# Kernel tuning notes

Measured on AMD Instinct MI355X. Metric: run time of the kernel, lower is better.

Reference implementation:

```python
import jax, jax.numpy as jnp
import numpy as np

M, IN, H, OUT, B = 64, 64, 256, 1, 4096


def setup_inputs() -> dict:
    key = jax.random.key(0)
    ks = jax.random.split(key, 7)
    s1 = 1.0 / np.sqrt(IN)
    s2 = 1.0 / np.sqrt(H)
    return {
        "xs": jax.random.normal(ks[0], (M, B, IN), dtype=jnp.float32),
        "W1": jax.random.uniform(ks[1], (M, IN, H), minval=-s1, maxval=s1, dtype=jnp.float32),
        "b1": jax.random.uniform(ks[2], (M, H), minval=-s1, maxval=s1, dtype=jnp.float32),
        "W2": jax.random.uniform(ks[3], (M, H, H), minval=-s2, maxval=s2, dtype=jnp.float32),
        "b2": jax.random.uniform(ks[4], (M, H), minval=-s2, maxval=s2, dtype=jnp.float32),
        "W3": jax.random.uniform(ks[5], (M, H, OUT), minval=-s2, maxval=s2, dtype=jnp.float32),
        "b3": jax.random.uniform(ks[6], (M, OUT), minval=-s2, maxval=s2, dtype=jnp.float32),
    }


def reference(xs, W1, b1, W2, b2, W3, b3):
    # Batched over models: [M, B, in] x [M, in, h] -> [M, B, h]
    h1 = jax.nn.relu(jnp.einsum("mbi,mih->mbh", xs, W1) + b1[:, None, :])
    h2 = jax.nn.relu(jnp.einsum("mbh,mhk->mbk", h1, W2) + b2[:, None, :])
    out = jnp.einsum("mbh,mho->mbo", h2, W3) + b3[:, None, :]
    return out  # [M, B, out]
```

## Files before the change

### kernel.cpp

```cpp
#include <hip/hip_runtime.h>

#define NMODELS 64
#define BBATCH  4096
#define IN_DIM  64
#define H_DIM   256

typedef __attribute__((ext_vector_type(8))) short short8;
typedef __attribute__((ext_vector_type(4))) short short4v;
typedef __attribute__((ext_vector_type(4))) float floatx4;

__device__ __forceinline__ unsigned short f2bf(float f) {
    unsigned int u = __builtin_bit_cast(unsigned int, f);
    return (unsigned short)((u + 0x8000u) >> 16);
}

__global__ __launch_bounds__(256) void prep_weights(const float* __restrict__ W1,
                                                    const float* __restrict__ W2,
                                                    unsigned short* __restrict__ w1t,
                                                    unsigned short* __restrict__ w2t) {
    __shared__ float lds[64][65];
    const int bid = blockIdx.x;
    const float* src;
    unsigned short* dst;
    int K, N, m, kb, nb;
    if (bid < 256) {
        m = bid >> 2; kb = 0; nb = bid & 3; K = IN_DIM; N = H_DIM;
        src = W1; dst = w1t;
    } else {
        int t = bid - 256;
        m = t >> 4; kb = (t >> 2) & 3; nb = t & 3; K = H_DIM; N = H_DIM;
        src = W2; dst = w2t;
    }
    const float* s = src + ((size_t)m * K + (size_t)kb * 64) * N + nb * 64;
    const int tid = threadIdx.x;
    const int r = tid >> 4, c4 = (tid & 15) * 4;
#pragma unroll
    for (int p = 0; p < 4; ++p) {
        int row = p * 16 + r;
        float4 v = *(const float4*)(s + (size_t)row * N + c4);
        lds[row][c4] = v.x; lds[row][c4 + 1] = v.y;
        lds[row][c4 + 2] = v.z; lds[row][c4 + 3] = v.w;
    }
    __syncthreads();
    unsigned short* dbase = dst + ((size_t)m * N + (size_t)nb * 64) * K + kb * 64;
    const int j = tid & 7;
#pragma unroll
    for (int it = 0; it < 2; ++it) {
        int n = it * 32 + (tid >> 3);
        unsigned short tmp[8];
#pragma unroll
        for (int e = 0; e < 8; ++e) tmp[e] = f2bf(lds[j * 8 + e][n]);
        *(short8*)(dbase + (size_t)n * K + j * 8) = *(const short8*)tmp;
    }
}

__global__ __launch_bounds__(256, 3) void mlp_fused(
    const float* __restrict__ xs,
    const unsigned short* __restrict__ w1t,
    const float* __restrict__ b1,
    const unsigned short* __restrict__ w2t,
    const float* __restrict__ b2,
    const float* __restrict__ w3,
    const float* __restrict__ b3,
    float* __restrict__ out)
{
    __shared__ unsigned short h1s[64 * 256];
    float* red = (float*)h1s;

    const int bid = blockIdx.x;
    const int m   = bid >> 6;
    const int tb  = bid & 63;
    const int tid = threadIdx.x;
    const int w   = tid >> 6;
    const int lane = tid & 63;
    const int q   = lane >> 4;
    const int c16 = lane & 15;
    const int sw  = c16 & 7;

    const float* xrow = xs + ((size_t)m * BBATCH + (size_t)tb * 64) * IN_DIM;
    const unsigned short* w1p = w1t + (size_t)m * (H_DIM * IN_DIM)
                                + (w * 64 + c16 * 4) * IN_DIM + q * 8;

    short8 ax[4][2];
#pragma unroll
    for (int rb = 0; rb < 4; ++rb)
#pragma unroll
        for (int kb = 0; kb < 2; ++kb) {
            const float* xp = xrow + (rb * 16 + c16) * IN_DIM + kb * 32 + q * 8;
            float4 v0 = *(const float4*)xp;
            float4 v1 = *(const float4*)(xp + 4);
            short8 a;
            a[0] = (short)f2bf(v0.x); a[1] = (short)f2bf(v0.y);
            a[2] = (short)f2bf(v0.z); a[3] = (short)f2bf(v0.w);
            a[4] = (short)f2bf(v1.x); a[5] = (short)f2bf(v1.y);
            a[6] = (short)f2bf(v1.z); a[7] = (short)f2bf(v1.w);
            ax[rb][kb] = a;
        }

    floatx4 acc[4][4];
#pragma unroll
    for (int rb = 0; rb < 4; ++rb)
#pragma unroll
        for (int nb = 0; nb < 4; ++nb)
            acc[rb][nb] = (floatx4){0.f, 0.f, 0.f, 0.f};

#pragma unroll
    for (int kb = 0; kb < 2; ++kb) {
        short8 bw[4];
#pragma unroll
        for (int nb = 0; nb < 4; ++nb)
            bw[nb] = *(const short8*)(w1p + nb * IN_DIM + kb * 32);
#pragma unroll
        for (int nb = 0; nb < 4; ++nb)
#pragma unroll
            for (int rb = 0; rb < 4; ++rb)
                acc[rb][nb] = __builtin_amdgcn_mfma_f32_16x16x32_bf16(
                    ax[rb][kb], bw[nb], acc[rb][nb], 0, 0, 0);
    }

    {
        floatx4 b1v = *(const floatx4*)(b1 + m * H_DIM + w * 64 + c16 * 4);
#pragma unroll
        for (int rb = 0; rb < 4; ++rb)
#pragma unroll
            for (int r = 0; r < 4; ++r) {
                short4v t;
#pragma unroll
                for (int nb = 0; nb < 4; ++nb)
                    t[nb] = (short)f2bf(fmaxf(acc[rb][nb][r] + b1v[nb], 0.f));
                int row = rb * 16 + q * 4 + r;
                int chunk = (w * 8 + (c16 >> 1)) ^ (row & 7);
                *(short4v*)((char*)h1s + row * 512 + chunk * 16 + (c16 & 1) * 8) = t;
            }
    }
    __syncthreads();

#pragma unroll
    for (int rb = 0; rb < 4; ++rb)
#pragma unroll
        for (int nb = 0; nb < 4; ++nb)
            acc[rb][nb] = (floatx4){0.f, 0.f, 0.f, 0.f};

    const unsigned short* w2p = w2t + (size_t)m * (H_DIM * H_DIM)
                                + (w * 64 + c16 * 4) * H_DIM + q * 8;
    short8 bvA[4], bvB[4];
#pragma unroll
    for (int nb = 0; nb < 4; ++nb)
        bvA[nb] = *(const short8*)(w2p + nb * H_DIM);
#pragma unroll
    for (int kb = 0; kb < 8; ++kb) {
        short8* cur = (kb & 1) ? bvB : bvA;
        short8* nxt = (kb & 1) ? bvA : bvB;
        if (kb < 7) {
#pragma unroll
            for (int nb = 0; nb < 4; ++nb)
                nxt[nb] = *(const short8*)(w2p + nb * H_DIM + (kb + 1) * 32);
        }
        short8 av[4];
#pragma unroll
        for (int rb = 0; rb < 4; ++rb)
            av[rb] = *(const short8*)((char*)h1s + (rb * 16 + c16) * 512
                                      + (((kb * 4 + q) ^ sw) * 16));
#pragma unroll
        for (int nb = 0; nb < 4; ++nb)
#pragma unroll
            for (int rb = 0; rb < 4; ++rb)
                acc[rb][nb] = __builtin_amdgcn_mfma_f32_16x16x32_bf16(
                    av[rb], cur[nb], acc[rb][nb], 0, 0, 0);
    }

    floatx4 b2v = *(const floatx4*)(b2 + m * H_DIM + w * 64 + c16 * 4);
    floatx4 w3v = *(const floatx4*)(w3 + m * H_DIM + w * 64 + c16 * 4);
    float p[4][4];
#pragma unroll
    for (int rb = 0; rb < 4; ++rb)
#pragma unroll
        for (int r = 0; r < 4; ++r) p[rb][r] = 0.f;
#pragma unroll
    for (int rb = 0; rb < 4; ++rb)
#pragma unroll
        for (int nb = 0; nb < 4; ++nb)
#pragma unroll
            for (int r = 0; r < 4; ++r) {
                float v = fmaxf(acc[rb][nb][r] + b2v[nb], 0.f);
                p[rb][r] += v * w3v[nb];
            }

    __syncthreads();
    const int unit = w * 16 + c16;
#pragma unroll
    for (int rb = 0; rb < 4; ++rb)
#pragma unroll
        for (int r = 0; r < 4; ++r)
            red[(rb * 16 + q * 4 + r) * 65 + unit] = p[rb][r];
    __syncthreads();
    if (tid < 64) {
        float s = b3[m];
#pragma unroll
        for (int u = 0; u < 64; ++u) s += red[tid * 65 + u];
        out[(size_t)m * BBATCH + tb * 64 + tid] = s;
    }
}

extern "C" void kernel_launch(void* const* d_in, const int* in_sizes, int n_in,
                              void* d_out, int out_size, void* d_ws, size_t ws_size,
                              hipStream_t stream) {
    const float* xs = (const float*)d_in[0];
    const float* W1 = (const float*)d_in[1];
    const float* b1 = (const float*)d_in[2];
    const float* W2 = (const float*)d_in[3];
    const float* b2 = (const float*)d_in[4];
    const float* W3 = (const float*)d_in[5];
    const float* b3 = (const float*)d_in[6];
    float* out = (float*)d_out;

    unsigned short* w1t = (unsigned short*)d_ws;
    unsigned short* w2t = w1t + (size_t)NMODELS * H_DIM * IN_DIM;

    prep_weights<<<256 + NMODELS * 16, 256, 0, stream>>>(W1, W2, w1t, w2t);
    mlp_fused<<<NMODELS * (BBATCH / 64), 256, 0, stream>>>(xs, w1t, b1, w2t, b2, W3, b3, out);
}
```

Measured before the change: 212.4 us.

## Process two batch tiles per block to reuse weight fragments, shuffle-reduce output

Each block now handles 128 batch rows (two 64-row tiles) per model, so every W1/W2 fragment loaded from global memory feeds twice as many MFMAs and the grid is halved. The final layer-3 reduction uses wave shuffles before a small LDS sum, and bf16 conversion uses the packed intrinsic. The explicit double-buffered W2 prefetch is dropped, LDS doubles to 64 KB, and occupancy drops to 2 blocks per CU with more accumulator registers.

```diff
diff --git a/kernel.cpp b/kernel.cpp
--- a/kernel.cpp
+++ b/kernel.cpp
@@ -1,4 +1,5 @@
 #include <hip/hip_runtime.h>
+#include <hip/hip_bf16.h>
 
 #define NMODELS 64
 #define BBATCH  4096
@@ -6,12 +7,19 @@
 #define H_DIM   256
 
 typedef __attribute__((ext_vector_type(8))) short short8;
-typedef __attribute__((ext_vector_type(4))) short short4v;
 typedef __attribute__((ext_vector_type(4))) float floatx4;
+typedef __attribute__((ext_vector_type(4))) unsigned int uint4v;
+typedef __attribute__((ext_vector_type(2))) unsigned int uint2v;
 
 __device__ __forceinline__ unsigned short f2bf(float f) {
     unsigned int u = __builtin_bit_cast(unsigned int, f);
     return (unsigned short)((u + 0x8000u) >> 16);
+}
+__device__ __forceinline__ unsigned int pkbf(float a, float b) {
+    __hip_bfloat162 h = __float22bfloat162_rn(make_float2(a, b));
+    unsigned int u;
+    __builtin_memcpy(&u, &h, 4);
+    return u;
 }
 
 __global__ __launch_bounds__(256) void prep_weights(const float* __restrict__ W1,
@@ -54,7 +62,7 @@
     }
 }
 
-__global__ __launch_bounds__(256, 3) void mlp_fused(
+__global__ __launch_bounds__(256, 2) void mlp_fused(
     const float* __restrict__ xs,
     const unsigned short* __restrict__ w1t,
     const float* __restrict__ b1,
@@ -64,12 +72,12 @@
     const float* __restrict__ b3,
     float* __restrict__ out)
 {
-    __shared__ unsigned short h1s[64 * 256];
+    __shared__ unsigned short h1s[2][64 * 256];
     float* red = (float*)h1s;
 
     const int bid = blockIdx.x;
-    const int m   = bid >> 6;
-    const int tb  = bid & 63;
+    const int m     = bid >> 5;
+    const int tile0 = (bid & 31) * 2;
     const int tid = threadIdx.x;
     const int w   = tid >> 6;
     const int lane = tid & 63;
@@ -77,128 +85,153 @@
     const int c16 = lane & 15;
     const int sw  = c16 & 7;
 
-    const float* xrow = xs + ((size_t)m * BBATCH + (size_t)tb * 64) * IN_DIM;
+    const float* xrow0 = xs + ((size_t)m * BBATCH + (size_t)tile0 * 64) * IN_DIM;
     const unsigned short* w1p = w1t + (size_t)m * (H_DIM * IN_DIM)
                                 + (w * 64 + c16 * 4) * IN_DIM + q * 8;
 
-    short8 ax[4][2];
-#pragma unroll
-    for (int rb = 0; rb < 4; ++rb)
-#pragma unroll
-        for (int kb = 0; kb < 2; ++kb) {
-            const float* xp = xrow + (rb * 16 + c16) * IN_DIM + kb * 32 + q * 8;
-            float4 v0 = *(const float4*)xp;
-            float4 v1 = *(const float4*)(xp + 4);
-            short8 a;
-            a[0] = (short)f2bf(v0.x); a[1] = (short)f2bf(v0.y);
-            a[2] = (short)f2bf(v0.z); a[3] = (short)f2bf(v0.w);
-            a[4] = (short)f2bf(v1.x); a[5] = (short)f2bf(v1.y);
-            a[6] = (short)f2bf(v1.z); a[7] = (short)f2bf(v1.w);
-            ax[rb][kb] = a;
-        }
-
-    floatx4 acc[4][4];
-#pragma unroll
-    for (int rb = 0; rb < 4; ++rb)
-#pragma unroll
-        for (int nb = 0; nb < 4; ++nb)
-            acc[rb][nb] = (floatx4){0.f, 0.f, 0.f, 0.f};
-
-#pragma unroll
-    for (int kb = 0; kb < 2; ++kb) {
-        short8 bw[4];
-#pragma unroll
-        for (int nb = 0; nb < 4; ++nb)
-            bw[nb] = *(const short8*)(w1p + nb * IN_DIM + kb * 32);
-#pragma unroll
-        for (int nb = 0; nb < 4; ++nb)
-#pragma unroll
-            for (int rb = 0; rb < 4; ++rb)
-                acc[rb][nb] = __builtin_amdgcn_mfma_f32_16x16x32_bf16(
-                    ax[rb][kb], bw[nb], acc[rb][nb], 0, 0, 0);
+    short8 ax[2][4][2];
+#pragma unroll
+    for (int t = 0; t < 2; ++t)
+#pragma unroll
+        for (int rb = 0; rb < 4; ++rb)
+#pragma unroll
+            for (int kb = 0; kb < 2; ++kb) {
+                const float* xp = xrow0 + (size_t)t * 64 * IN_DIM
+                                  + (rb * 16 + c16) * IN_DIM + kb * 32 + q * 8;
+                float4 v0 = *(const float4*)xp;
+                float4 v1 = *(const float4*)(xp + 4);
+                uint4v u;
+                u[0] = pkbf(v0.x, v0.y); u[1] = pkbf(v0.z, v0.w);
+                u[2] = pkbf(v1.x, v1.y); u[3] = pkbf(v1.z, v1.w);
+                ax[t][rb][kb] = __builtin_bit_cast(short8, u);
+            }
+
+    floatx4 acc[2][4][4];
+#pragma unroll
+    for (int t = 0; t < 2; ++t)
+#pragma unroll
+        for (int rb = 0; rb < 4; ++rb)
+#pragma unroll
+            for (int nb = 0; nb < 4; ++nb)
+                acc[t][rb][nb] = (floatx4){0.f, 0.f, 0.f, 0.f};
+
+    {
+        short8 bw[2][4];
+#pragma unroll
+        for (int kb = 0; kb < 2; ++kb)
+#pragma unroll
+            for (int nb = 0; nb < 4; ++nb)
+                bw[kb][nb] = *(const short8*)(w1p + nb * IN_DIM + kb * 32);
+#pragma unroll
+        for (int t = 0; t < 2; ++t)
+#pragma unroll
+            for (int kb = 0; kb < 2; ++kb)
+#pragma unroll
+                for (int nb = 0; nb < 4; ++nb)
+#pragma unroll
+                    for (int rb = 0; rb < 4; ++rb)
+                        acc[t][rb][nb] = __builtin_amdgcn_mfma_f32_16x16x32_bf16(
+                            ax[t][rb][kb], bw[kb][nb], acc[t][rb][nb], 0, 0, 0);
     }
 
     {
         floatx4 b1v = *(const floatx4*)(b1 + m * H_DIM + w * 64 + c16 * 4);
 #pragma unroll
-        for (int rb = 0; rb < 4; ++rb)
-#pragma unroll
-            for (int r = 0; r < 4; ++r) {
-                short4v t;
-#pragma unroll
-                for (int nb = 0; nb < 4; ++nb)
-                    t[nb] = (short)f2bf(fmaxf(acc[rb][nb][r] + b1v[nb], 0.f));
-                int row = rb * 16 + q * 4 + r;
-                int chunk = (w * 8 + (c16 >> 1)) ^ (row & 7);
-                *(short4v*)((char*)h1s + row * 512 + chunk * 16 + (c16 & 1) * 8) = t;
-            }
-    }
-    __syncthreads();
-
-#pragma unroll
-    for (int rb = 0; rb < 4; ++rb)
-#pragma unroll
-        for (int nb = 0; nb < 4; ++nb)
-            acc[rb][nb] = (floatx4){0.f, 0.f, 0.f, 0.f};
+        for (int t = 0; t < 2; ++t)
+#pragma unroll
+            for (int rb = 0; rb < 4; ++rb)
+#pragma unroll
+                for (int r = 0; r < 4; ++r) {
+                    float v0 = fmaxf(acc[t][rb][0][r] + b1v[0], 0.f);
+                    float v1 = fmaxf(acc[t][rb][1][r] + b1v[1], 0.f);
+                    float v2 = fmaxf(acc[t][rb][2][r] + b1v[2], 0.f);
+                    float v3 = fmaxf(acc[t][rb][3][r] + b1v[3], 0.f);
+                    uint2v u; u[0] = pkbf(v0, v1); u[1] = pkbf(v2, v3);
+                    int row = rb * 16 + q * 4 + r;
+                    int chunk = (w * 8 + (c16 >> 1)) ^ (row & 7);
+                    *(uint2v*)((char*)&h1s[t][0] + row * 512 + chunk * 16 + (c16 & 1) * 8) = u;
+                }
+    }
+    __syncthreads();
+
+#pragma unroll
+    for (int t = 0; t < 2; ++t)
+#pragma unroll
+        for (int rb = 0; rb < 4; ++rb)
+#pragma unroll
+            for (int nb = 0; nb < 4; ++nb)
+                acc[t][rb][nb] = (floatx4){0.f, 0.f, 0.f, 0.f};
 
     const unsigned short* w2p = w2t + (size_t)m * (H_DIM * H_DIM)
                                 + (w * 64 + c16 * 4) * H_DIM + q * 8;
-    short8 bvA[4], bvB[4];
-#pragma unroll
-    for (int nb = 0; nb < 4; ++nb)
-        bvA[nb] = *(const short8*)(w2p + nb * H_DIM);
 #pragma unroll
     for (int kb = 0; kb < 8; ++kb) {
-        short8* cur = (kb & 1) ? bvB : bvA;
-        short8* nxt = (kb & 1) ? bvA : bvB;
-        if (kb < 7) {
-#pragma unroll
-            for (int nb = 0; nb < 4; ++nb)
-                nxt[nb] = *(const short8*)(w2p + nb * H_DIM + (kb + 1) * 32);
-        }
-        short8 av[4];
-#pragma unroll
-        for (int rb = 0; rb < 4; ++rb)
-            av[rb] = *(const short8*)((char*)h1s + (rb * 16 + c16) * 512
-                                      + (((kb * 4 + q) ^ sw) * 16));
+        short8 bv[4], av[2][4];
 #pragma unroll
         for (int nb = 0; nb < 4; ++nb)
-#pragma unroll
-            for (int rb = 0; rb < 4; ++rb)
-                acc[rb][nb] = __builtin_amdgcn_mfma_f32_16x16x32_bf16(
-                    av[rb], cur[nb], acc[rb][nb], 0, 0, 0);
+            bv[nb] = *(const short8*)(w2p + nb * H_DIM + kb * 32);
+#pragma unroll
+        for (int t = 0; t < 2; ++t)
+#pragma unroll
+            for (int rb = 0; rb < 4; ++rb)
+                av[t][rb] = *(const short8*)((char*)&h1s[t][0] + (rb * 16 + c16) * 512
+                                             + (((kb * 4 + q) ^ sw) * 16));
+#pragma unroll
+        for (int nb = 0; nb < 4; ++nb)
+#pragma unroll
+            for (int t = 0; t < 2; ++t)
+#pragma unroll
+                for (int rb = 0; rb < 4; ++rb)
+                    acc[t][rb][nb] = __builtin_amdgcn_mfma_f32_16x16x32_bf16(
+                        av[t][rb], bv[nb], acc[t][rb][nb], 0, 0, 0);
     }
 
     floatx4 b2v = *(const floatx4*)(b2 + m * H_DIM + w * 64 + c16 * 4);
     floatx4 w3v = *(const floatx4*)(w3 + m * H_DIM + w * 64 + c16 * 4);
-    float p[4][4];
-#pragma unroll
-    for (int rb = 0; rb < 4; ++rb)
-#pragma unroll
-        for (int r = 0; r < 4; ++r) p[rb][r] = 0.f;
-#pragma unroll
-    for (int rb = 0; rb < 4; ++rb)
-#pragma unroll
-        for (int nb = 0; nb < 4; ++nb)
-#pragma unroll
-            for (int r = 0; r < 4; ++r) {
-                float v = fmaxf(acc[rb][nb][r] + b2v[nb], 0.f);
-                p[rb][r] += v * w3v[nb];
-            }
-
-    __syncthreads();
-    const int unit = w * 16 + c16;
-#pragma unroll
-    for (int rb = 0; rb < 4; ++rb)
-#pragma unroll
-        for (int r = 0; r < 4; ++r)
-            red[(rb * 16 + q * 4 + r) * 65 + unit] = p[rb][r];
-    __syncthreads();
-    if (tid < 64) {
-        float s = b3[m];
-#pragma unroll
-        for (int u = 0; u < 64; ++u) s += red[tid * 65 + u];
-        out[(size_t)m * BBATCH + tb * 64 + tid] = s;
+    float p[2][4][4];
+#pragma unroll
+    for (int t = 0; t < 2; ++t)
+#pragma unroll
+        for (int rb = 0; rb < 4; ++rb)
+#pragma unroll
+            for (int r = 0; r < 4; ++r) p[t][rb][r] = 0.f;
+#pragma unroll
+    for (int t = 0; t < 2; ++t)
+#pragma unroll
+        for (int rb = 0; rb < 4; ++rb)
+#pragma unroll
+            for (int nb = 0; nb < 4; ++nb)
+#pragma unroll
+                for (int r = 0; r < 4; ++r) {
+                    float v = fmaxf(acc[t][rb][nb][r] + b2v[nb], 0.f);
+                    p[t][rb][r] += v * w3v[nb];
+                }
+#pragma unroll
+    for (int off = 1; off < 16; off <<= 1)
+#pragma unroll
+        for (int t = 0; t < 2; ++t)
+#pragma unroll
+            for (int rb = 0; rb < 4; ++rb)
+#pragma unroll
+                for (int r = 0; r < 4; ++r)
+                    p[t][rb][r] += __shfl_xor(p[t][rb][r], off);
+
+    __syncthreads();
+    if (c16 == 0) {
+#pragma unroll
+        for (int t = 0; t < 2; ++t)
+#pragma unroll
+            for (int rb = 0; rb < 4; ++rb)
+#pragma unroll
+                for (int r = 0; r < 4; ++r)
+                    red[t * 256 + w * 64 + rb * 16 + q * 4 + r] = p[t][rb][r];
+    }
+    __syncthreads();
+    if (tid < 128) {
+        int t = tid >> 6, rr = tid & 63;
+        const float* rt = red + t * 256;
+        float s = rt[rr] + rt[64 + rr] + rt[128 + rr] + rt[192 + rr] + b3[m];
+        out[(size_t)m * BBATCH + (tile0 + t) * 64 + rr] = s;
     }
 }
 
@@ -218,5 +251,5 @@
     unsigned short* w2t = w1t + (size_t)NMODELS * H_DIM * IN_DIM;
 
     prep_weights<<<256 + NMODELS * 16, 256, 0, stream>>>(W1, W2, w1t, w2t);
-    mlp_fused<<<NMODELS * (BBATCH / 64), 256, 0, stream>>>(xs, w1t, b1, w2t, b2, W3, b3, out);
-}
+    mlp_fused<<<NMODELS * (BBATCH / 128), 256, 0, stream>>>(xs, w1t, b1, w2t, b2, W3, b3, out);
+}
```

Measured after the change: 181.2 us. -14.7%, faster.
